# Kernel tuning notes

Measured on AMD Instinct MI355X. Metric: run time of the kernel, lower is better.

## Reference

```python
import jax, jax.numpy as jnp
import numpy as np

IO, H, S, N = 64, 1024, 512, 64

def setup_inputs() -> dict:
    key = jax.random.key(0)
    ks = jax.random.split(key, 6)
    scale = 0.05  # keep activations in a sane range for tanh/softmax
    return {
        "states": jax.random.normal(ks[0], (N, S, H), jnp.float32) * scale,
        "output_set": jax.random.normal(ks[1], (IO, H), jnp.float32) * scale,
        "Wo": jax.random.normal(ks[2], (2 * H, H), jnp.float32) * scale,
        "bo": jax.random.normal(ks[3], (H,), jnp.float32) * scale,
        "Wc": jax.random.normal(ks[4], (IO * H, IO), jnp.float32) * scale,
        "bc": jax.random.normal(ks[5], (IO,), jnp.float32) * scale,
    }

def reference(states, output_set, Wo, bo, Wc, bc):
    # Batched over the n_states Python loop of the original module.
    # attn scores: output_set [io,h] x states [n,s,h] -> [n,io,s]
    attn = jnp.einsum('ih,nsh->nis', output_set, states)
    attn = jax.nn.softmax(attn, axis=-1)  # softmax over context (sm_over_context=True)
    mix = jnp.einsum('nis,nsh->nih', attn, states)            # [n,io,h]
    out = jnp.broadcast_to(output_set[None], mix.shape)       # [n,io,h]
    combined = jnp.concatenate([mix, out], axis=-1)           # [n,io,2h]
    o = combined @ Wo + bo                                    # linear_out: 2h -> h
    logits = jnp.tanh(o).reshape(o.shape[0], -1) @ Wc + bc    # C: io*h -> io
    return logits
```

## Files before the change

kernel.cpp:

```cpp
#include <hip/hip_runtime.h>
#include <hip/hip_bf16.h>

#define IOdim 64
#define Hdim  1024
#define Sdim  512
#define Nbat  64

typedef __bf16 bf16x8_t __attribute__((ext_vector_type(8)));
typedef float  f32x4_t  __attribute__((ext_vector_type(4)));

#define MFMA16(a, b, c) __builtin_amdgcn_mfma_f32_16x16x32_bf16((a), (b), (c), 0, 0, 0)

__device__ __forceinline__ unsigned short f2bf(float f) {
    return __builtin_bit_cast(unsigned short, (__bf16)f);
}
__device__ __forceinline__ bf16x8_t cvt8(float4 p0, float4 p1) {
    bf16x8_t b;
    b[0] = (__bf16)p0.x; b[1] = (__bf16)p0.y; b[2] = (__bf16)p0.z; b[3] = (__bf16)p0.w;
    b[4] = (__bf16)p1.x; b[5] = (__bf16)p1.y; b[6] = (__bf16)p1.z; b[7] = (__bf16)p1.w;
    return b;
}
__device__ __forceinline__ void async16(const void* g, void* l) {
    __builtin_amdgcn_global_load_lds(
        (const __attribute__((address_space(1))) void*)g,
        (__attribute__((address_space(3))) void*)l, 16, 0, 0);
}

__global__ __launch_bounds__(256) void cvt_kernel(const float* __restrict__ in,
                                                  unsigned short* __restrict__ outp,
                                                  int nElem) {
    int idx = blockIdx.x * 256 + threadIdx.x;
    if (idx < nElem) outp[idx] = f2bf(in[idx]);
}

__global__ __launch_bounds__(256) void transpose_cvt(const float* __restrict__ in,
                                                     unsigned short* __restrict__ outp,
                                                     int R, int C) {
    __shared__ float tile[32][33];
    int c0 = blockIdx.x * 32, r0 = blockIdx.y * 32;
    int tx = threadIdx.x, ty = threadIdx.y;
#pragma unroll
    for (int i = 0; i < 4; i++) {
        int r = ty + i * 8;
        tile[r][tx] = in[(size_t)(r0 + r) * C + c0 + tx];
    }
    __syncthreads();
#pragma unroll
    for (int i = 0; i < 4; i++) {
        int r = ty + i * 8;
        outp[(size_t)(c0 + r) * R + r0 + tx] = f2bf(tile[tx][r]);
    }
}

__global__ __launch_bounds__(256) void scores_kernel(const float* __restrict__ states,
                                                     const unsigned short* __restrict__ osb,
                                                     float* __restrict__ attnf) {
    __shared__ float Bst[64 * 64];
    __shared__ unsigned short Ast[64 * 64];
    int n = blockIdx.y, s0 = blockIdx.x * 64;
    int tid = threadIdx.x, lane = tid & 63, w = tid >> 6;
    int col = lane & 15, quad = lane >> 4;
    const float* bsrc = states + ((size_t)(n * Sdim + s0 + (tid >> 4)) << 10) + (tid & 15) * 4;
    const unsigned short* asrc = osb + ((size_t)(tid >> 3) << 10) + (tid & 7) * 8;
    float* bdst = Bst + tid * 4;
    unsigned short* adst = Ast + tid * 8;
    f32x4_t acc[4] = {};
    for (int kc = 0; kc < Hdim; kc += 64) {
#pragma unroll
        for (int j = 0; j < 4; j++)
            async16(bsrc + ((size_t)j << 14) + kc, bdst + j * 1024);
#pragma unroll
        for (int j = 0; j < 2; j++)
            async16(asrc + ((size_t)j << 15) + kc, adst + j * 2048);
        __syncthreads();
#pragma unroll
        for (int kk = 0; kk < 2; kk++) {
            const float* bp = Bst + (w * 16 + col) * 64 + kk * 32 + quad * 8;
            float4 f0 = *(const float4*)bp;
            float4 f1 = *(const float4*)(bp + 4);
            bf16x8_t bfrag = cvt8(f0, f1);
#pragma unroll
            for (int a = 0; a < 4; a++) {
                bf16x8_t afrag = *(const bf16x8_t*)(Ast + (a * 16 + col) * 64 + kk * 32 + quad * 8);
                acc[a] = MFMA16(afrag, bfrag, acc[a]);
            }
        }
        __syncthreads();
    }
    float* ob = attnf + (size_t)(n * IOdim) * Sdim + s0 + w * 16 + col;
#pragma unroll
    for (int a = 0; a < 4; a++)
#pragma unroll
        for (int r = 0; r < 4; r++) {
            int i = a * 16 + quad * 4 + r;
            ob[(size_t)i * Sdim] = acc[a][r];
        }
}

__global__ __launch_bounds__(256) void softmax_kernel(const float* __restrict__ attnf,
                                                      unsigned short* __restrict__ attnb) {
    int row = blockIdx.x * 4 + (threadIdx.x >> 6);
    int lane = threadIdx.x & 63;
    const float* p = attnf + (size_t)row * Sdim + lane * 8;
    float4 v0 = ((const float4*)p)[0];
    float4 v1 = ((const float4*)p)[1];
    float v[8] = {v0.x, v0.y, v0.z, v0.w, v1.x, v1.y, v1.z, v1.w};
    float m = v[0];
#pragma unroll
    for (int j = 1; j < 8; j++) m = fmaxf(m, v[j]);
#pragma unroll
    for (int off = 32; off > 0; off >>= 1) m = fmaxf(m, __shfl_xor(m, off));
    float sum = 0.f;
#pragma unroll
    for (int j = 0; j < 8; j++) { v[j] = __expf(v[j] - m); sum += v[j]; }
#pragma unroll
    for (int off = 32; off > 0; off >>= 1) sum += __shfl_xor(sum, off);
    float inv = 1.0f / sum;
    union { unsigned short u[8]; uint4 q; } res;
#pragma unroll
    for (int j = 0; j < 8; j++) res.u[j] = f2bf(v[j] * inv);
    *(uint4*)(attnb + (size_t)row * Sdim + lane * 8) = res.q;
}

__global__ __launch_bounds__(256) void mix_kernel(const float* __restrict__ states,
                                                  const unsigned short* __restrict__ attnb,
                                                  unsigned short* __restrict__ mixb) {
    __shared__ unsigned short Tlds[64 * 72];
    int n = blockIdx.y, h0 = blockIdx.x * 64;
    int tid = threadIdx.x, lane = tid & 63, g = tid >> 6;
    int col = lane & 15, quad = lane >> 4;
    f32x4_t acc0 = {0,0,0,0}, acc1 = {0,0,0,0}, acc2 = {0,0,0,0}, acc3 = {0,0,0,0};
    const unsigned short* ap = attnb + (size_t)(n * IOdim + col) * Sdim + quad * 8;
    const float* sbase = states + (size_t)n * Sdim * Hdim + h0 + lane;
    float cur[16];
#pragma unroll
    for (int rep = 0; rep < 16; rep++) cur[rep] = sbase[(size_t)(g * 16 + rep) * Hdim];
    for (int sc = 0; sc < Sdim; sc += 64) {
        union { unsigned short u[16]; uint4 q[2]; } pk;
#pragma unroll
        for (int rep = 0; rep < 16; rep++) pk.u[rep] = f2bf(cur[rep]);
        if (sc) __syncthreads();
        *(uint4*)(Tlds + lane * 72 + g * 16)     = pk.q[0];
        *(uint4*)(Tlds + lane * 72 + g * 16 + 8) = pk.q[1];
        if (sc + 64 < Sdim) {
#pragma unroll
            for (int rep = 0; rep < 16; rep++)
                cur[rep] = sbase[(size_t)(sc + 64 + g * 16 + rep) * Hdim];
        }
        __syncthreads();
#pragma unroll
        for (int ks = 0; ks < 64; ks += 32) {
            bf16x8_t b  = *(const bf16x8_t*)(Tlds + (g * 16 + col) * 72 + ks + quad * 8);
            bf16x8_t a0 = *(const bf16x8_t*)(ap + sc + ks);
            bf16x8_t a1 = *(const bf16x8_t*)(ap + 16 * Sdim + sc + ks);
            bf16x8_t a2 = *(const bf16x8_t*)(ap + 32 * Sdim + sc + ks);
            bf16x8_t a3 = *(const bf16x8_t*)(ap + 48 * Sdim + sc + ks);
            acc0 = MFMA16(a0, b, acc0);
            acc1 = MFMA16(a1, b, acc1);
            acc2 = MFMA16(a2, b, acc2);
            acc3 = MFMA16(a3, b, acc3);
        }
    }
    f32x4_t accs[4] = {acc0, acc1, acc2, acc3};
    int h = h0 + g * 16 + col;
#pragma unroll
    for (int ai = 0; ai < 4; ai++)
#pragma unroll
        for (int r = 0; r < 4; r++) {
            int i = ai * 16 + quad * 4 + r;
            mixb[(size_t)(n * IOdim + i) * Hdim + h] = f2bf(accs[ai][r]);
        }
}

__global__ __launch_bounds__(256) void out_gemm(const unsigned short* __restrict__ mixb,
                                                const unsigned short* __restrict__ osb,
                                                const unsigned short* __restrict__ woT,
                                                const float* __restrict__ bo,
                                                unsigned short* __restrict__ tb) {
    __shared__ unsigned short Ald[128 * 32];
    __shared__ unsigned short Bld[64 * 32];
    int h0 = blockIdx.x * 64, r0 = blockIdx.y * 128;
    int tid = threadIdx.x, lane = tid & 63, w = tid >> 6;
    int col = lane & 15, quad = lane >> 4;
    int wx = w & 1, wy = w >> 1;
    int rowX = tid >> 2, seg = tid & 3;
    f32x4_t acc[4][2] = {};
    const unsigned short* m1 = mixb + (size_t)(r0 + rowX) * Hdim + seg * 8;
    const unsigned short* m2 = mixb + (size_t)(r0 + rowX + 64) * Hdim + seg * 8;
    const unsigned short* o1 = osb + (size_t)rowX * Hdim + seg * 8;
    const unsigned short* w1 = woT + (size_t)(h0 + rowX) * 2048 + seg * 8;
    unsigned short* lA1 = Ald + (size_t)tid * 8;
    unsigned short* lA2 = Ald + (size_t)(tid + 256) * 8;
    unsigned short* lB1 = Bld + (size_t)tid * 8;
    for (int kc = 0; kc < 2048; kc += 32) {
        if (kc < 1024) {
            async16(m1 + kc, lA1);
            async16(m2 + kc, lA2);
        } else {
            int k2 = kc - 1024;
            async16(o1 + k2, lA1);
            async16(o1 + k2, lA2);
        }
        async16(w1 + kc, lB1);
        __syncthreads();
        bf16x8_t af[4], bfr[2];
#pragma unroll
        for (int mi = 0; mi < 4; mi++)
            af[mi] = *(const bf16x8_t*)(Ald + (wy * 64 + mi * 16 + col) * 32 + quad * 8);
#pragma unroll
        for (int ni = 0; ni < 2; ni++)
            bfr[ni] = *(const bf16x8_t*)(Bld + (wx * 32 + ni * 16 + col) * 32 + quad * 8);
#pragma unroll
        for (int mi = 0; mi < 4; mi++)
#pragma unroll
            for (int ni = 0; ni < 2; ni++)
                acc[mi][ni] = MFMA16(af[mi], bfr[ni], acc[mi][ni]);
        __syncthreads();
    }
#pragma unroll
    for (int ni = 0; ni < 2; ni++) {
        int h = h0 + wx * 32 + ni * 16 + col;
        float bov = bo[h];
#pragma unroll
        for (int mi = 0; mi < 4; mi++)
#pragma unroll
            for (int r = 0; r < 4; r++) {
                int rr = r0 + wy * 64 + mi * 16 + quad * 4 + r;
                tb[(size_t)rr * Hdim + h] = f2bf(tanhf(acc[mi][ni][r] + bov));
            }
    }
}

__global__ __launch_bounds__(256) void final_gemm(const unsigned short* __restrict__ tb,
                                                  const unsigned short* __restrict__ wcT,
                                                  float* __restrict__ partials) {
    int kc0 = blockIdx.x * 128;
    int tid = threadIdx.x, lane = tid & 63, g = tid >> 6;
    int col = lane & 15, quad = lane >> 4;
    f32x4_t acc0 = {0,0,0,0}, acc1 = {0,0,0,0}, acc2 = {0,0,0,0}, acc3 = {0,0,0,0};
    const unsigned short* ap = tb + (size_t)col * 65536 + kc0 + quad * 8;
    const unsigned short* bp = wcT + (size_t)(g * 16 + col) * 65536 + kc0 + quad * 8;
    bf16x8_t B[2], A0[2], A1[2], A2[2], A3[2];
#pragma unroll
    for (int t = 0; t < 2; t++) {
        B[t]  = *(const bf16x8_t*)(bp + t * 32);
        A0[t] = *(const bf16x8_t*)(ap + t * 32);
        A1[t] = *(const bf16x8_t*)(ap + (size_t)16 * 65536 + t * 32);
        A2[t] = *(const bf16x8_t*)(ap + (size_t)32 * 65536 + t * 32);
        A3[t] = *(const bf16x8_t*)(ap + (size_t)48 * 65536 + t * 32);
    }
#pragma unroll
    for (int c = 0; c < 4; c++) {
        int p = c & 1;
        acc0 = MFMA16(A0[p], B[p], acc0);
        acc1 = MFMA16(A1[p], B[p], acc1);
        acc2 = MFMA16(A2[p], B[p], acc2);
        acc3 = MFMA16(A3[p], B[p], acc3);
        if (c + 2 < 4) {
            int kn = (c + 2) * 32;
            B[p]  = *(const bf16x8_t*)(bp + kn);
            A0[p] = *(const bf16x8_t*)(ap + kn);
            A1[p] = *(const bf16x8_t*)(ap + (size_t)16 * 65536 + kn);
            A2[p] = *(const bf16x8_t*)(ap + (size_t)32 * 65536 + kn);
            A3[p] = *(const bf16x8_t*)(ap + (size_t)48 * 65536 + kn);
        }
    }
    f32x4_t accs[4] = {acc0, acc1, acc2, acc3};
    int j = g * 16 + col;
    float* pb = partials + blockIdx.x * 4096;
#pragma unroll
    for (int ai = 0; ai < 4; ai++)
#pragma unroll
        for (int r = 0; r < 4; r++) {
            int nn = ai * 16 + quad * 4 + r;
            pb[nn * 64 + j] = accs[ai][r];
        }
}

__global__ __launch_bounds__(256) void reduce_kernel(const float* __restrict__ partials,
                                                     const float* __restrict__ bc,
                                                     float* __restrict__ out) {
    int idx = blockIdx.x * 256 + threadIdx.x;
    float s = bc[idx & 63];
#pragma unroll 8
    for (int b = 0; b < 512; b++) s += partials[b * 4096 + idx];
    out[idx] = s;
}

extern "C" void kernel_launch(void* const* d_in, const int* in_sizes, int n_in,
                              void* d_out, int out_size, void* d_ws, size_t ws_size,
                              hipStream_t stream) {
    const float* states     = (const float*)d_in[0];
    const float* output_set = (const float*)d_in[1];
    const float* Wo         = (const float*)d_in[2];
    const float* bo         = (const float*)d_in[3];
    const float* Wc         = (const float*)d_in[4];
    const float* bc         = (const float*)d_in[5];
    float* out = (float*)d_out;

    char* ws = (char*)d_ws;
    float*          attnf = (float*)ws;
    float*          parts = (float*)ws;
    unsigned short* attnb = (unsigned short*)(ws + (8u  << 20));
    unsigned short* mixb  = (unsigned short*)(ws + (12u << 20));
    unsigned short* tb    = (unsigned short*)(ws + (20u << 20));
    unsigned short* woT   = (unsigned short*)(ws + (28u << 20));
    unsigned short* osb   = (unsigned short*)(ws + (32u << 20));
    unsigned short* wcT   = (unsigned short*)(ws + (32u << 20) + (1u << 18));

    cvt_kernel<<<dim3(IOdim * Hdim / 256), dim3(256), 0, stream>>>(output_set, osb, IOdim * Hdim);
    transpose_cvt<<<dim3(Hdim / 32, 2048 / 32), dim3(32, 8), 0, stream>>>(Wo, woT, 2048, Hdim);
    transpose_cvt<<<dim3(64 / 32, 65536 / 32), dim3(32, 8), 0, stream>>>(Wc, wcT, 65536, 64);
    scores_kernel<<<dim3(Sdim / 64, Nbat), dim3(256), 0, stream>>>(states, osb, attnf);
    softmax_kernel<<<dim3(Nbat * IOdim / 4), dim3(256), 0, stream>>>(attnf, attnb);
    mix_kernel<<<dim3(Hdim / 64, Nbat), dim3(256), 0, stream>>>(states, attnb, mixb);
    out_gemm<<<dim3(Hdim / 64, Nbat * IOdim / 128), dim3(256), 0, stream>>>(mixb, osb, woT, bo, tb);
    final_gemm<<<dim3(512), dim3(256), 0, stream>>>(tb, wcT, parts);
    reduce_kernel<<<dim3(16), dim3(256), 0, stream>>>(parts, bc, out);
}
```

Before: 340.7 us.

## Precompute output_set half of linear_out once and swizzle LDS in GEMMs

```diff
diff --git a/kernel.cpp b/kernel.cpp
--- a/kernel.cpp
+++ b/kernel.cpp
@@ -50,6 +50,34 @@
         int r = ty + i * 8;
         outp[(size_t)(c0 + r) * R + r0 + tx] = f2bf(tile[tx][r]);
     }
+}
+
+__global__ __launch_bounds__(256) void ob_kernel(const unsigned short* __restrict__ osb,
+                                                 const unsigned short* __restrict__ woT,
+                                                 const float* __restrict__ bo,
+                                                 float* __restrict__ ob) {
+    int h0 = blockIdx.x * 64;
+    int tid = threadIdx.x, lane = tid & 63, w = tid >> 6;
+    int col = lane & 15, quad = lane >> 4;
+    f32x4_t acc[4] = {};
+    const unsigned short* bp  = woT + (size_t)(h0 + w * 16 + col) * 2048 + 1024 + quad * 8;
+    const unsigned short* apb = osb + (size_t)col * 1024 + quad * 8;
+    for (int kc = 0; kc < 1024; kc += 32) {
+        bf16x8_t bfrag = *(const bf16x8_t*)(bp + kc);
+#pragma unroll
+        for (int a = 0; a < 4; a++) {
+            bf16x8_t afrag = *(const bf16x8_t*)(apb + (size_t)a * 16 * 1024 + kc);
+            acc[a] = MFMA16(bfrag, afrag, acc[a]);
+        }
+    }
+#pragma unroll
+    for (int a = 0; a < 4; a++)
+#pragma unroll
+        for (int r = 0; r < 4; r++) {
+            int i = a * 16 + col;
+            int h = h0 + w * 16 + quad * 4 + r;
+            ob[(size_t)i * Hdim + h] = acc[a][r] + bo[h];
+        }
 }
 
 __global__ __launch_bounds__(256) void scores_kernel(const float* __restrict__ states,
@@ -60,10 +88,13 @@
     int n = blockIdx.y, s0 = blockIdx.x * 64;
     int tid = threadIdx.x, lane = tid & 63, w = tid >> 6;
     int col = lane & 15, quad = lane >> 4;
-    const float* bsrc = states + ((size_t)(n * Sdim + s0 + (tid >> 4)) << 10) + (tid & 15) * 4;
-    const unsigned short* asrc = osb + ((size_t)(tid >> 3) << 10) + (tid & 7) * 8;
+    const float* bsrc = states + ((size_t)(n * Sdim + s0 + (tid >> 4)) << 10)
+                      + (((tid & 15) ^ ((tid >> 4) & 7)) << 2);
+    const unsigned short* asrc = osb + ((size_t)(tid >> 3) << 10)
+                      + (((tid & 7) ^ ((tid >> 3) & 7)) << 3);
     float* bdst = Bst + tid * 4;
     unsigned short* adst = Ast + tid * 8;
+    int xs = col & 7;
     f32x4_t acc[4] = {};
     for (int kc = 0; kc < Hdim; kc += 64) {
 #pragma unroll
@@ -75,25 +106,27 @@
         __syncthreads();
 #pragma unroll
         for (int kk = 0; kk < 2; kk++) {
-            const float* bp = Bst + (w * 16 + col) * 64 + kk * 32 + quad * 8;
-            float4 f0 = *(const float4*)bp;
-            float4 f1 = *(const float4*)(bp + 4);
+            int R = w * 16 + col;
+            int sg = kk * 8 + quad * 2;
+            float4 f0 = *(const float4*)(Bst + R * 64 + ((sg ^ xs) << 2));
+            float4 f1 = *(const float4*)(Bst + R * 64 + (((sg + 1) ^ xs) << 2));
             bf16x8_t bfrag = cvt8(f0, f1);
 #pragma unroll
             for (int a = 0; a < 4; a++) {
-                bf16x8_t afrag = *(const bf16x8_t*)(Ast + (a * 16 + col) * 64 + kk * 32 + quad * 8);
+                bf16x8_t afrag = *(const bf16x8_t*)(Ast + (a * 16 + col) * 64
+                                                    + (((kk * 4 + quad) ^ xs) << 3));
                 acc[a] = MFMA16(afrag, bfrag, acc[a]);
             }
         }
         __syncthreads();
     }
-    float* ob = attnf + (size_t)(n * IOdim) * Sdim + s0 + w * 16 + col;
+    float* obp = attnf + (size_t)(n * IOdim) * Sdim + s0 + w * 16 + col;
 #pragma unroll
     for (int a = 0; a < 4; a++)
 #pragma unroll
         for (int r = 0; r < 4; r++) {
             int i = a * 16 + quad * 4 + r;
-            ob[(size_t)i * Sdim] = acc[a][r];
+            obp[(size_t)i * Sdim] = acc[a][r];
         }
 }
 
@@ -173,60 +206,58 @@
 }
 
 __global__ __launch_bounds__(256) void out_gemm(const unsigned short* __restrict__ mixb,
-                                                const unsigned short* __restrict__ osb,
                                                 const unsigned short* __restrict__ woT,
-                                                const float* __restrict__ bo,
+                                                const float* __restrict__ ob,
                                                 unsigned short* __restrict__ tb) {
-    __shared__ unsigned short Ald[128 * 32];
-    __shared__ unsigned short Bld[64 * 32];
+    __shared__ unsigned short Ald[128 * 64];
+    __shared__ unsigned short Bld[64 * 64];
     int h0 = blockIdx.x * 64, r0 = blockIdx.y * 128;
     int tid = threadIdx.x, lane = tid & 63, w = tid >> 6;
     int col = lane & 15, quad = lane >> 4;
     int wx = w & 1, wy = w >> 1;
-    int rowX = tid >> 2, seg = tid & 3;
+    int sw = ((tid & 7) ^ ((tid >> 3) & 7)) * 8;
+    const unsigned short* m1 = mixb + (size_t)(r0 + (tid >> 3)) * Hdim + sw;
+    const unsigned short* w1 = woT + (size_t)(h0 + (tid >> 3)) * 2048 + sw;
+    unsigned short* lA = Ald + (size_t)tid * 8;
+    unsigned short* lB = Bld + (size_t)tid * 8;
+    int xs = col & 7;
     f32x4_t acc[4][2] = {};
-    const unsigned short* m1 = mixb + (size_t)(r0 + rowX) * Hdim + seg * 8;
-    const unsigned short* m2 = mixb + (size_t)(r0 + rowX + 64) * Hdim + seg * 8;
-    const unsigned short* o1 = osb + (size_t)rowX * Hdim + seg * 8;
-    const unsigned short* w1 = woT + (size_t)(h0 + rowX) * 2048 + seg * 8;
-    unsigned short* lA1 = Ald + (size_t)tid * 8;
-    unsigned short* lA2 = Ald + (size_t)(tid + 256) * 8;
-    unsigned short* lB1 = Bld + (size_t)tid * 8;
-    for (int kc = 0; kc < 2048; kc += 32) {
-        if (kc < 1024) {
-            async16(m1 + kc, lA1);
-            async16(m2 + kc, lA2);
-        } else {
-            int k2 = kc - 1024;
-            async16(o1 + k2, lA1);
-            async16(o1 + k2, lA2);
-        }
-        async16(w1 + kc, lB1);
-        __syncthreads();
-        bf16x8_t af[4], bfr[2];
-#pragma unroll
-        for (int mi = 0; mi < 4; mi++)
-            af[mi] = *(const bf16x8_t*)(Ald + (wy * 64 + mi * 16 + col) * 32 + quad * 8);
-#pragma unroll
-        for (int ni = 0; ni < 2; ni++)
-            bfr[ni] = *(const bf16x8_t*)(Bld + (wx * 32 + ni * 16 + col) * 32 + quad * 8);
-#pragma unroll
-        for (int mi = 0; mi < 4; mi++)
+    for (int kc = 0; kc < 1024; kc += 64) {
+#pragma unroll
+        for (int j = 0; j < 4; j++)
+            async16(m1 + (size_t)j * 32 * Hdim + kc, lA + j * 2048);
+#pragma unroll
+        for (int j = 0; j < 2; j++)
+            async16(w1 + (size_t)j * 32 * 2048 + kc, lB + j * 2048);
+        __syncthreads();
+#pragma unroll
+        for (int kk = 0; kk < 2; kk++) {
+            bf16x8_t bfr[2];
 #pragma unroll
             for (int ni = 0; ni < 2; ni++)
-                acc[mi][ni] = MFMA16(af[mi], bfr[ni], acc[mi][ni]);
+                bfr[ni] = *(const bf16x8_t*)(Bld + (wx * 32 + ni * 16 + col) * 64
+                                             + (((kk * 4 + quad) ^ xs) << 3));
+#pragma unroll
+            for (int mi = 0; mi < 4; mi++) {
+                bf16x8_t af = *(const bf16x8_t*)(Ald + (wy * 64 + mi * 16 + col) * 64
+                                                 + (((kk * 4 + quad) ^ xs) << 3));
+#pragma unroll
+                for (int ni = 0; ni < 2; ni++)
+                    acc[mi][ni] = MFMA16(af, bfr[ni], acc[mi][ni]);
+            }
+        }
         __syncthreads();
     }
 #pragma unroll
     for (int ni = 0; ni < 2; ni++) {
         int h = h0 + wx * 32 + ni * 16 + col;
-        float bov = bo[h];
 #pragma unroll
         for (int mi = 0; mi < 4; mi++)
 #pragma unroll
             for (int r = 0; r < 4; r++) {
                 int rr = r0 + wy * 64 + mi * 16 + quad * 4 + r;
-                tb[(size_t)rr * Hdim + h] = f2bf(tanhf(acc[mi][ni][r] + bov));
+                int i = rr & 63;
+                tb[(size_t)rr * Hdim + h] = f2bf(tanhf(acc[mi][ni][r] + ob[(size_t)i * Hdim + h]));
             }
     }
 }
@@ -280,11 +311,16 @@
 __global__ __launch_bounds__(256) void reduce_kernel(const float* __restrict__ partials,
                                                      const float* __restrict__ bc,
                                                      float* __restrict__ out) {
-    int idx = blockIdx.x * 256 + threadIdx.x;
-    float s = bc[idx & 63];
-#pragma unroll 8
-    for (int b = 0; b < 512; b++) s += partials[b * 4096 + idx];
-    out[idx] = s;
+    __shared__ float red[4][64];
+    int tid = threadIdx.x, lane = tid & 63, w = tid >> 6;
+    int idx = blockIdx.x * 64 + lane;
+    float s = 0.f;
+#pragma unroll 4
+    for (int c = w; c < 512; c += 4) s += partials[(size_t)c * 4096 + idx];
+    red[w][lane] = s;
+    __syncthreads();
+    if (w == 0)
+        out[idx] = red[0][lane] + red[1][lane] + red[2][lane] + red[3][lane] + bc[idx & 63];
 }
 
 extern "C" void kernel_launch(void* const* d_in, const int* in_sizes, int n_in,
@@ -307,14 +343,16 @@
     unsigned short* woT   = (unsigned short*)(ws + (28u << 20));
     unsigned short* osb   = (unsigned short*)(ws + (32u << 20));
     unsigned short* wcT   = (unsigned short*)(ws + (32u << 20) + (1u << 18));
+    float*          obuf  = (float*)(ws + (40u << 20) + (1u << 18));
 
     cvt_kernel<<<dim3(IOdim * Hdim / 256), dim3(256), 0, stream>>>(output_set, osb, IOdim * Hdim);
     transpose_cvt<<<dim3(Hdim / 32, 2048 / 32), dim3(32, 8), 0, stream>>>(Wo, woT, 2048, Hdim);
     transpose_cvt<<<dim3(64 / 32, 65536 / 32), dim3(32, 8), 0, stream>>>(Wc, wcT, 65536, 64);
+    ob_kernel<<<dim3(Hdim / 64), dim3(256), 0, stream>>>(osb, woT, bo, obuf);
     scores_kernel<<<dim3(Sdim / 64, Nbat), dim3(256), 0, stream>>>(states, osb, attnf);
     softmax_kernel<<<dim3(Nbat * IOdim / 4), dim3(256), 0, stream>>>(attnf, attnb);
     mix_kernel<<<dim3(Hdim / 64, Nbat), dim3(256), 0, stream>>>(states, attnb, mixb);
-    out_gemm<<<dim3(Hdim / 64, Nbat * IOdim / 128), dim3(256), 0, stream>>>(mixb, osb, woT, bo, tb);
+    out_gemm<<<dim3(Hdim / 64, Nbat * IOdim / 128), dim3(256), 0, stream>>>(mixb, woT, obuf, tb);
     final_gemm<<<dim3(512), dim3(256), 0, stream>>>(tb, wcT, parts);
-    reduce_kernel<<<dim3(16), dim3(256), 0, stream>>>(parts, bc, out);
-}
+    reduce_kernel<<<dim3(64), dim3(256), 0, stream>>>(parts, bc, out);
+}
```

Result: no change. 334.8 us (-1.7%).
